# Performance work log

Measured on AMD Instinct MI355X. Metric: run time of the kernel, lower is better.

The kernel has to match this reference:

```python
import jax, jax.numpy as jnp
import numpy as np

T, D, H, L = 4096, 1024, 512, 2  # seq_len, input_size, per-direction hidden (state_size//2), num_layers


def setup_inputs() -> dict:
    key = jax.random.key(0)
    inp = {"emb": jax.random.normal(key, (T, D), jnp.float32) * 0.1}
    k = 1
    for d in ("fwd", "bwd"):
        for l in range(L):
            in_sz = D if l == 0 else H
            inp[f"{d}_Wih_{l}"] = jax.random.normal(jax.random.fold_in(key, k), (4 * H, in_sz), jnp.float32) * float(1.0 / np.sqrt(in_sz)); k += 1
            inp[f"{d}_Whh_{l}"] = jax.random.normal(jax.random.fold_in(key, k), (4 * H, H), jnp.float32) * float(1.0 / np.sqrt(H)); k += 1
            inp[f"{d}_bih_{l}"] = jnp.zeros((4 * H,), jnp.float32)
            inp[f"{d}_bhh_{l}"] = jnp.zeros((4 * H,), jnp.float32)
    return inp


def _lstm_stack(xs, params):
    """Run a stack of unidirectional LSTM layers over xs [T, in].
    Returns (final cells [L,H], final hiddens [L,H], top-layer outputs [T,H])."""
    cTs, hTs = [], []
    for Wih, Whh, bih, bhh in params:
        h0 = jnp.zeros((Wih.shape[0] // 4,), xs.dtype)

        def step(carry, x, Wih=Wih, Whh=Whh, b=bih + bhh):
            h, c = carry
            g = Wih @ x + Whh @ h + b          # [4H], torch LSTMCell gate order i,f,g,o
            i, f, gg, o = jnp.split(g, 4)
            c = jax.nn.sigmoid(f) * c + jax.nn.sigmoid(i) * jnp.tanh(gg)
            h = jax.nn.sigmoid(o) * jnp.tanh(c)
            return (h, c), h

        (hT, cT), xs = jax.lax.scan(step, (h0, h0), xs)
        cTs.append(cT)
        hTs.append(hT)
    return jnp.stack(cTs), jnp.stack(hTs), xs


def reference(emb,
              fwd_Wih_0, fwd_Whh_0, fwd_bih_0, fwd_bhh_0,
              fwd_Wih_1, fwd_Whh_1, fwd_bih_1, fwd_bhh_1,
              bwd_Wih_0, bwd_Whh_0, bwd_bih_0, bwd_bhh_0,
              bwd_Wih_1, bwd_Whh_1, bwd_bih_1, bwd_bhh_1):
    fparams = [(fwd_Wih_0, fwd_Whh_0, fwd_bih_0, fwd_bhh_0),
               (fwd_Wih_1, fwd_Whh_1, fwd_bih_1, fwd_bhh_1)]
    bparams = [(bwd_Wih_0, bwd_Whh_0, bwd_bih_0, bwd_bhh_0),
               (bwd_Wih_1, bwd_Whh_1, bwd_bih_1, bwd_bhh_1)]
    fc, fh, fy = _lstm_stack(emb, fparams)          # forward pass over sequence
    bc, bh, by = _lstm_stack(emb[::-1], bparams)    # backward pass over reversed sequence
    cell_memories = jnp.concatenate([fc, bc], axis=-1)   # [L, state_size]
    hidden_states = jnp.concatenate([fh, bh], axis=-1)   # [L, state_size]
    outputs = jnp.concatenate([fy, by[::-1]], axis=-1)   # [T, state_size] per-token final-layer states
    return (cell_memories, hidden_states, outputs)
```

## Files before the change

### kernel.cpp

```cpp
#include <hip/hip_runtime.h>
#include <cstdint>
#include <cstddef>

#define T_SEQ 4096
#define HSZ   512
#define NGATE 2048
#define DIN   1024
#define NB0   16
#define HB0   32
#define NB1   32
#define HB1   16
#define S_SLOT 16
#define CH    132

typedef unsigned long long u64;
typedef unsigned int u32;

__device__ __forceinline__ u64 exld(const u64* p) {
  return __hip_atomic_load(p, __ATOMIC_RELAXED, __HIP_MEMORY_SCOPE_AGENT);
}
__device__ __forceinline__ void exst(u64* p, u64 v) {
  __hip_atomic_store(p, v, __ATOMIC_RELAXED, __HIP_MEMORY_SCOPE_AGENT);
}
__device__ __forceinline__ int pgld(const u32* p) {
  return (int)__hip_atomic_load(p, __ATOMIC_RELAXED, __HIP_MEMORY_SCOPE_AGENT);
}
__device__ __forceinline__ void pgst(u32* p, u32 v) {
  __hip_atomic_store(p, v, __ATOMIC_RELAXED, __HIP_MEMORY_SCOPE_AGENT);
}

__device__ __forceinline__ float frcp(float x) { return __builtin_amdgcn_rcpf(x); }
__device__ __forceinline__ float fsig(float x) { return frcp(1.f + __expf(-x)); }
__device__ __forceinline__ float ftnh(float x) { return 1.f - 2.f * frcp(1.f + __expf(2.f * x)); }

__global__ void init_sync_kernel(u64* ex, u32* prog) {
  const int tid = blockIdx.x * blockDim.x + threadIdx.x;
  if (tid < 2 * 2 * S_SLOT * HSZ) exst(&ex[tid], 0ull);
  if (tid < 2 * (NB0 + NB1)) pgst(&prog[tid], 0u);
}

__global__ __launch_bounds__(256, 2)
void gemm_bias_kernel(const float* __restrict__ Xf, const float* __restrict__ Xb,
                      const float* __restrict__ Wf, const float* __restrict__ Wb,
                      const float* __restrict__ bif, const float* __restrict__ bhf,
                      const float* __restrict__ bib, const float* __restrict__ bhb,
                      float* __restrict__ Pf, float* __restrict__ Pb, int K)
{
  const int dir = blockIdx.z;
  const float* X  = dir ? Xb  : Xf;
  const float* W  = dir ? Wb  : Wf;
  const float* bi = dir ? bib : bif;
  const float* bh = dir ? bhb : bhf;
  float* P        = dir ? Pb  : Pf;

  const int m0 = blockIdx.x * 128;
  const int n0 = blockIdx.y * 128;
  const int tid = threadIdx.x;
  const int lr = tid >> 1;
  const int lk = (tid & 1) * 8;

  __shared__ float As[16*128];
  __shared__ float Bs[16*128];

  float acc[8][8];
  #pragma unroll
  for (int i = 0; i < 8; ++i)
    #pragma unroll
    for (int j = 0; j < 8; ++j) acc[i][j] = 0.f;

  for (int k0 = 0; k0 < K; k0 += 16) {
    const float4 a0 = *(const float4*)(X + (size_t)(m0+lr)*K + k0 + lk);
    const float4 a1 = *(const float4*)(X + (size_t)(m0+lr)*K + k0 + lk + 4);
    const float4 b0 = *(const float4*)(W + (size_t)(n0+lr)*K + k0 + lk);
    const float4 b1 = *(const float4*)(W + (size_t)(n0+lr)*K + k0 + lk + 4);
    __syncthreads();
    As[(lk+0)*128+lr]=a0.x; As[(lk+1)*128+lr]=a0.y; As[(lk+2)*128+lr]=a0.z; As[(lk+3)*128+lr]=a0.w;
    As[(lk+4)*128+lr]=a1.x; As[(lk+5)*128+lr]=a1.y; As[(lk+6)*128+lr]=a1.z; As[(lk+7)*128+lr]=a1.w;
    Bs[(lk+0)*128+lr]=b0.x; Bs[(lk+1)*128+lr]=b0.y; Bs[(lk+2)*128+lr]=b0.z; Bs[(lk+3)*128+lr]=b0.w;
    Bs[(lk+4)*128+lr]=b1.x; Bs[(lk+5)*128+lr]=b1.y; Bs[(lk+6)*128+lr]=b1.z; Bs[(lk+7)*128+lr]=b1.w;
    __syncthreads();
    #pragma unroll
    for (int kk = 0; kk < 16; ++kk) {
      const float4 A0 = *(const float4*)(As + kk*128 + (tid&15)*8);
      const float4 A1 = *(const float4*)(As + kk*128 + (tid&15)*8 + 4);
      const float4 B0 = *(const float4*)(Bs + kk*128 + (tid>>4)*8);
      const float4 B1 = *(const float4*)(Bs + kk*128 + (tid>>4)*8 + 4);
      const float av[8] = {A0.x,A0.y,A0.z,A0.w,A1.x,A1.y,A1.z,A1.w};
      const float bv[8] = {B0.x,B0.y,B0.z,B0.w,B1.x,B1.y,B1.z,B1.w};
      #pragma unroll
      for (int i = 0; i < 8; ++i)
        #pragma unroll
        for (int j = 0; j < 8; ++j) acc[i][j] += av[i]*bv[j];
    }
  }
  const int tm = m0 + (tid&15)*8;
  const int tn = n0 + (tid>>4)*8;
  #pragma unroll
  for (int i = 0; i < 8; ++i) {
    #pragma unroll
    for (int j = 0; j < 8; ++j) {
      const int n = tn + j;
      P[(size_t)(tm+i)*NGATE + n] = acc[i][j] + bi[n] + bh[n];
    }
  }
}

__global__ __launch_bounds__(512, 2)
void fused_recur_kernel(const float* __restrict__ Whh0_f, const float* __restrict__ Whh0_b,
                        const float* __restrict__ Wih1_f, const float* __restrict__ Whh1_f,
                        const float* __restrict__ bih1_f, const float* __restrict__ bhh1_f,
                        const float* __restrict__ Wih1_b, const float* __restrict__ Whh1_b,
                        const float* __restrict__ bih1_b, const float* __restrict__ bhh1_b,
                        const float* __restrict__ P_f, const float* __restrict__ P_b,
                        u64* ex0, u64* ex1, u32* prog0, u32* prog1,
                        float* __restrict__ out)
{
  const int bx  = blockIdx.x;
  const int tid = threadIdx.x;
  const int lane = tid & 63;
  const int wv   = tid >> 6;

  __shared__ float xh[2][8*CH];

  if (bx < 2*NB0) {
    const int dir = (bx >= NB0) ? 1 : 0;
    const int b   = bx - dir*NB0;
    const float* Whh = dir ? Whh0_b : Whh0_f;
    const float* P   = dir ? P_b    : P_f;
    u64* exS   = ex0 + (size_t)dir*S_SLOT*HSZ;
    u32* prS   = prog0 + dir*NB0;
    u32* prL1  = prog1 + dir*NB1;

    const int g  = lane & 3;
    const int el = (lane >> 2) & 3;
    const int cc = lane >> 4;
    const int e  = wv*4 + el;
    const int grow = g*HSZ + b*HB0 + e;
    const bool red0 = (cc == 0);
    const bool pub  = red0 && (g == 0);

    float4 w[32];
    {
      const float4* wp = (const float4*)(Whh + (size_t)grow*HSZ + cc*128);
      #pragma unroll
      for (int j = 0; j < 32; ++j) w[j] = wp[j];
    }

    float creg = 0.f;
    float pv = 0.f;
    if (red0) pv = P[(size_t)(dir ? (T_SEQ-1) : 0)*NGATE + grow];

    for (int t = 0; t < T_SEQ; ++t) {
      if ((t & 7) == 0) {
        if (tid >= 64 && tid < 64+NB0)       { while (pgld(&prS[tid-64])  < t-4) {} }
        else if (tid >= 96 && tid < 96+NB1)  { while (pgld(&prL1[tid-96]) < t-4) {} }
      }
      {
        const u64* sp = exS + (size_t)(t & (S_SLOT-1))*HSZ + tid;
        u64 v;
        do { v = exld(sp); } while ((u32)(v >> 32) != (u32)t);
        xh[t & 1][(tid>>7)*CH + (tid & 127)] = __uint_as_float((u32)v);
      }
      __syncthreads();
      if (tid == 0) pgst(&prS[b], (u32)(t+1));
      float pvn = 0.f;
      if (red0 && t+1 < T_SEQ) pvn = P[(size_t)(dir ? (T_SEQ-2-t) : (t+1))*NGATE + grow];
      const float4* h4 = (const float4*)(xh[t & 1] + cc*CH);
      float a0=0.f, a1=0.f, a2=0.f, a3=0.f;
      #pragma unroll
      for (int j = 0; j < 32; j += 4) {
        const float4 h0 = h4[j], h1 = h4[j+1], h2 = h4[j+2], h3 = h4[j+3];
        a0 += w[j].x*h0.x   + w[j].y*h0.y   + w[j].z*h0.z   + w[j].w*h0.w;
        a1 += w[j+1].x*h1.x + w[j+1].y*h1.y + w[j+1].z*h1.z + w[j+1].w*h1.w;
        a2 += w[j+2].x*h2.x + w[j+2].y*h2.y + w[j+2].z*h2.z + w[j+2].w*h2.w;
        a3 += w[j+3].x*h3.x + w[j+3].y*h3.y + w[j+3].z*h3.z + w[j+3].w*h3.w;
      }
      float acc = (a0+a1)+(a2+a3);
      acc += __shfl_xor(acc, 16);
      acc += __shfl_xor(acc, 32);
      const float val = acc + pv;
      pv = pvn;
      const float av = (g == 2) ? ftnh(val) : fsig(val);
      const float f1 = __shfl_xor(av, 1);
      const float f2 = __shfl_xor(av, 2);
      const float f3 = __shfl_xor(av, 3);
      if (pub) {
        creg = f1*creg + av*f2;
        const float hnew = f3*ftnh(creg);
        const int hidx = b*HB0 + e;
        const u64 pkt = ((u64)(u32)(t+1) << 32) | (u64)__float_as_uint(hnew);
        exst(exS + (size_t)((t+1) & (S_SLOT-1))*HSZ + hidx, pkt);
        if (t == T_SEQ-1) {
          out[dir*HSZ + hidx]        = creg;
          out[2048 + dir*HSZ + hidx] = hnew;
        }
      }
    }
  } else {
    const int r   = bx - 2*NB0;
    const int dir = (r >= NB1) ? 1 : 0;
    const int b   = r - dir*NB1;
    const float* Wih = dir ? Wih1_b : Wih1_f;
    const float* Whh = dir ? Whh1_b : Whh1_f;
    const float* bi  = dir ? bih1_b : bih1_f;
    const float* bh  = dir ? bhh1_b : bhh1_f;
    u64* exX = ex0 + (size_t)dir*S_SLOT*HSZ;
    u64* exS = ex1 + (size_t)dir*S_SLOT*HSZ;
    u32* prS = prog1 + dir*NB1;

    const int g   = lane & 3;
    const int el  = (lane >> 2) & 1;
    const int sub = lane >> 3;
    const int e   = wv*2 + el;
    const int grow = g*HSZ + b*HB1 + e;
    const bool red0 = (sub == 0);
    const bool pub  = red0 && (g == 0);

    float4 w[32];
    {
      const float* wsrc = (sub < 4) ? (Wih + (size_t)grow*HSZ + sub*128)
                                    : (Whh + (size_t)grow*HSZ + (sub-4)*128);
      const float4* wp = (const float4*)wsrc;
      #pragma unroll
      for (int j = 0; j < 32; ++j) w[j] = wp[j];
    }
    float brow = 0.f;
    if (red0) brow = bi[grow] + bh[grow];

    float creg = 0.f;
    u64 xpf = exld(exX + (size_t)(1 & (S_SLOT-1))*HSZ + tid);

    for (int t = 0; t < T_SEQ; ++t) {
      if ((t & 7) == 0 && tid >= 64 && tid < 64+NB1) { while (pgld(&prS[tid-64]) < t-4) {} }
      {
        const u64* px = exX + (size_t)((t+1) & (S_SLOT-1))*HSZ + tid;
        const u64* ph = exS + (size_t)(t & (S_SLOT-1))*HSZ + tid;
        u64 vx = xpf; bool okx = ((u32)(vx >> 32) == (u32)(t+1));
        float hv = 0.f; bool okh = false;
        do {
          if (!okx) { u64 v = exld(px); if ((u32)(v >> 32) == (u32)(t+1)) { vx = v; okx = true; } }
          if (!okh) { u64 v = exld(ph); if ((u32)(v >> 32) == (u32)t)     { hv = __uint_as_float((u32)v); okh = true; } }
        } while (!(okx && okh));
        xh[t & 1][(tid>>7)*CH + (tid & 127)]       = __uint_as_float((u32)vx);
        xh[t & 1][(4 + (tid>>7))*CH + (tid & 127)] = hv;
      }
      __syncthreads();
      if (tid == 0) pgst(&prS[b], (u32)(t+1));
      xpf = exld(exX + (size_t)((t+2) & (S_SLOT-1))*HSZ + tid);
      const float4* v4 = (const float4*)(xh[t & 1] + sub*CH);
      float a0=0.f, a1=0.f, a2=0.f, a3=0.f;
      #pragma unroll
      for (int j = 0; j < 32; j += 4) {
        const float4 h0 = v4[j], h1 = v4[j+1], h2 = v4[j+2], h3 = v4[j+3];
        a0 += w[j].x*h0.x   + w[j].y*h0.y   + w[j].z*h0.z   + w[j].w*h0.w;
        a1 += w[j+1].x*h1.x + w[j+1].y*h1.y + w[j+1].z*h1.z + w[j+1].w*h1.w;
        a2 += w[j+2].x*h2.x + w[j+2].y*h2.y + w[j+2].z*h2.z + w[j+2].w*h2.w;
        a3 += w[j+3].x*h3.x + w[j+3].y*h3.y + w[j+3].z*h3.z + w[j+3].w*h3.w;
      }
      float acc = (a0+a1)+(a2+a3);
      acc += __shfl_xor(acc, 8);
      acc += __shfl_xor(acc, 16);
      acc += __shfl_xor(acc, 32);
      const float val = acc + brow;
      const float av = (g == 2) ? ftnh(val) : fsig(val);
      const float f1 = __shfl_xor(av, 1);
      const float f2 = __shfl_xor(av, 2);
      const float f3 = __shfl_xor(av, 3);
      if (pub) {
        creg = f1*creg + av*f2;
        const float hnew = f3*ftnh(creg);
        const int hidx = b*HB1 + e;
        const u64 pkt = ((u64)(u32)(t+1) << 32) | (u64)__float_as_uint(hnew);
        exst(exS + (size_t)((t+1) & (S_SLOT-1))*HSZ + hidx, pkt);
        const int trow = dir ? (T_SEQ-1-t) : t;
        out[4096 + (size_t)trow*1024 + dir*HSZ + hidx] = hnew;
        if (t == T_SEQ-1) {
          out[1024 + dir*HSZ + hidx]        = creg;
          out[2048 + 1024 + dir*HSZ + hidx] = hnew;
        }
      }
    }
  }
}

extern "C" void kernel_launch(void* const* d_in, const int* in_sizes, int n_in,
                              void* d_out, int out_size, void* d_ws, size_t ws_size,
                              hipStream_t stream)
{
  const float* emb   = (const float*)d_in[0];
  const float* fWih0 = (const float*)d_in[1];
  const float* fWhh0 = (const float*)d_in[2];
  const float* fbih0 = (const float*)d_in[3];
  const float* fbhh0 = (const float*)d_in[4];
  const float* fWih1 = (const float*)d_in[5];
  const float* fWhh1 = (const float*)d_in[6];
  const float* fbih1 = (const float*)d_in[7];
  const float* fbhh1 = (const float*)d_in[8];
  const float* bWih0 = (const float*)d_in[9];
  const float* bWhh0 = (const float*)d_in[10];
  const float* bbih0 = (const float*)d_in[11];
  const float* bbhh0 = (const float*)d_in[12];
  const float* bWih1 = (const float*)d_in[13];
  const float* bWhh1 = (const float*)d_in[14];
  const float* bbih1 = (const float*)d_in[15];
  const float* bbhh1 = (const float*)d_in[16];
  float* out = (float*)d_out;

  float* P_f = (float*)d_ws;
  float* P_b = P_f + (size_t)T_SEQ*NGATE;
  u64*   ex0 = (u64*)(P_b + (size_t)T_SEQ*NGATE);
  u64*   ex1 = ex0 + 2*S_SLOT*HSZ;
  u32*   prog0 = (u32*)(ex1 + 2*S_SLOT*HSZ);
  u32*   prog1 = prog0 + 2*NB0;

  init_sync_kernel<<<32, 1024, 0, stream>>>(ex0, prog0);

  gemm_bias_kernel<<<dim3(32,16,2), 256, 0, stream>>>(
      emb, emb, fWih0, bWih0, fbih0, fbhh0, bbih0, bbhh0, P_f, P_b, DIN);

  fused_recur_kernel<<<96, 512, 0, stream>>>(
      fWhh0, bWhh0,
      fWih1, fWhh1, fbih1, fbhh1,
      bWih1, bWhh1, bbih1, bbhh1,
      P_f, P_b, ex0, ex1, prog0, prog1, out);
}
```

Before: 7.998 ms.

## Poll exchange buffers with wide 16-byte loads from fewer waves

Each polling thread now reads four tagged hidden-state values with dwordx4 inline-asm loads (sc0 sc1, cache-bypassing) instead of one 64-bit atomic load per thread. Polling is confined to the first 128 or 256 threads, so other waves skip it, and the progress-flag wait and publish move to wave 4. A fallback reverts to per-element atomic loads if 2048 wide-load attempts fail, since a 16-byte load is not guaranteed to be atomic. Launch bounds drop to one block per SM and an empty asm pins the weights in registers, trading occupancy for no register spills; the L1 next-step prefetch of x is removed.

```diff
diff --git a/kernel.cpp b/kernel.cpp
--- a/kernel.cpp
+++ b/kernel.cpp
@@ -27,6 +27,49 @@
 }
 __device__ __forceinline__ void pgst(u32* p, u32 v) {
   __hip_atomic_store(p, v, __ATOMIC_RELAXED, __HIP_MEMORY_SCOPE_AGENT);
+}
+
+__device__ __forceinline__ ulonglong2 exld16(const u64* p) {
+  ulonglong2 v;
+  asm volatile("global_load_dwordx4 %0, %1, off sc0 sc1\n"
+               "s_waitcnt vmcnt(0)"
+               : "=&v"(v) : "v"(p) : "memory");
+  return v;
+}
+__device__ __forceinline__ void exld16x2(const u64* p, ulonglong2& A, ulonglong2& B) {
+  asm volatile("global_load_dwordx4 %0, %2, off sc0 sc1\n"
+               "global_load_dwordx4 %1, %2, off offset:16 sc0 sc1\n"
+               "s_waitcnt vmcnt(0)"
+               : "=&v"(A), "=&v"(B) : "v"(p) : "memory");
+}
+
+__device__ __forceinline__ void poll4(const u64* base, u32 tag, bool& fast, float4& out) {
+  if (fast) {
+    ulonglong2 A, B; bool okA = false, okB = false; int it = 0;
+    while (!(okA && okB)) {
+      ulonglong2 nA, nB;
+      if (!okA && !okB) exld16x2(base, nA, nB);
+      else if (!okA)    nA = exld16(base);
+      else              nB = exld16(base + 2);
+      if (!okA && (u32)(nA.x >> 32) == tag && (u32)(nA.y >> 32) == tag) { A = nA; okA = true; }
+      if (!okB && (u32)(nB.x >> 32) == tag && (u32)(nB.y >> 32) == tag) { B = nB; okB = true; }
+      if (++it > 2048) { fast = false; break; }
+    }
+    if (okA && okB) {
+      out = make_float4(__uint_as_float((u32)A.x), __uint_as_float((u32)A.y),
+                        __uint_as_float((u32)B.x), __uint_as_float((u32)B.y));
+      return;
+    }
+  }
+  u64 v0=0, v1=0, v2=0, v3=0; bool o0=false, o1=false, o2=false, o3=false;
+  while (!(o0 && o1 && o2 && o3)) {
+    if (!o0) { u64 v = exld(base+0); if ((u32)(v>>32) == tag) { v0 = v; o0 = true; } }
+    if (!o1) { u64 v = exld(base+1); if ((u32)(v>>32) == tag) { v1 = v; o1 = true; } }
+    if (!o2) { u64 v = exld(base+2); if ((u32)(v>>32) == tag) { v2 = v; o2 = true; } }
+    if (!o3) { u64 v = exld(base+3); if ((u32)(v>>32) == tag) { v3 = v; o3 = true; } }
+  }
+  out = make_float4(__uint_as_float((u32)v0), __uint_as_float((u32)v1),
+                    __uint_as_float((u32)v2), __uint_as_float((u32)v3));
 }
 
 __device__ __forceinline__ float frcp(float x) { return __builtin_amdgcn_rcpf(x); }
@@ -105,7 +148,7 @@
   }
 }
 
-__global__ __launch_bounds__(512, 2)
+__global__ __launch_bounds__(512, 1)
 void fused_recur_kernel(const float* __restrict__ Whh0_f, const float* __restrict__ Whh0_b,
                         const float* __restrict__ Wih1_f, const float* __restrict__ Whh1_f,
                         const float* __restrict__ bih1_f, const float* __restrict__ bhh1_f,
@@ -145,24 +188,27 @@
       #pragma unroll
       for (int j = 0; j < 32; ++j) w[j] = wp[j];
     }
+    #pragma unroll
+    for (int j = 0; j < 32; ++j)
+      asm volatile("" : "+v"(w[j].x), "+v"(w[j].y), "+v"(w[j].z), "+v"(w[j].w));
 
     float creg = 0.f;
     float pv = 0.f;
     if (red0) pv = P[(size_t)(dir ? (T_SEQ-1) : 0)*NGATE + grow];
+    bool fastH = true;
 
     for (int t = 0; t < T_SEQ; ++t) {
       if ((t & 7) == 0) {
-        if (tid >= 64 && tid < 64+NB0)       { while (pgld(&prS[tid-64])  < t-4) {} }
-        else if (tid >= 96 && tid < 96+NB1)  { while (pgld(&prL1[tid-96]) < t-4) {} }
-      }
-      {
-        const u64* sp = exS + (size_t)(t & (S_SLOT-1))*HSZ + tid;
-        u64 v;
-        do { v = exld(sp); } while ((u32)(v >> 32) != (u32)t);
-        xh[t & 1][(tid>>7)*CH + (tid & 127)] = __uint_as_float((u32)v);
+        if (tid >= 256 && tid < 256+NB0)      { while (pgld(&prS[tid-256])  < t-4) {} }
+        else if (tid >= 288 && tid < 288+NB1) { while (pgld(&prL1[tid-288]) < t-4) {} }
+      }
+      if (tid < 128) {
+        float4 hv4;
+        poll4(exS + (size_t)(t & (S_SLOT-1))*HSZ + 4*tid, (u32)t, fastH, hv4);
+        *(float4*)&xh[t & 1][(tid>>5)*CH + 4*(tid&31)] = hv4;
       }
       __syncthreads();
-      if (tid == 0) pgst(&prS[b], (u32)(t+1));
+      if (tid == 256) pgst(&prS[b], (u32)(t+1));
       float pvn = 0.f;
       if (red0 && t+1 < T_SEQ) pvn = P[(size_t)(dir ? (T_SEQ-2-t) : (t+1))*NGATE + grow];
       const float4* h4 = (const float4*)(xh[t & 1] + cc*CH);
@@ -224,29 +270,30 @@
       #pragma unroll
       for (int j = 0; j < 32; ++j) w[j] = wp[j];
     }
+    #pragma unroll
+    for (int j = 0; j < 32; ++j)
+      asm volatile("" : "+v"(w[j].x), "+v"(w[j].y), "+v"(w[j].z), "+v"(w[j].w));
+
     float brow = 0.f;
     if (red0) brow = bi[grow] + bh[grow];
 
     float creg = 0.f;
-    u64 xpf = exld(exX + (size_t)(1 & (S_SLOT-1))*HSZ + tid);
+    bool fastX = true, fastH = true;
 
     for (int t = 0; t < T_SEQ; ++t) {
-      if ((t & 7) == 0 && tid >= 64 && tid < 64+NB1) { while (pgld(&prS[tid-64]) < t-4) {} }
-      {
-        const u64* px = exX + (size_t)((t+1) & (S_SLOT-1))*HSZ + tid;
-        const u64* ph = exS + (size_t)(t & (S_SLOT-1))*HSZ + tid;
-        u64 vx = xpf; bool okx = ((u32)(vx >> 32) == (u32)(t+1));
-        float hv = 0.f; bool okh = false;
-        do {
-          if (!okx) { u64 v = exld(px); if ((u32)(v >> 32) == (u32)(t+1)) { vx = v; okx = true; } }
-          if (!okh) { u64 v = exld(ph); if ((u32)(v >> 32) == (u32)t)     { hv = __uint_as_float((u32)v); okh = true; } }
-        } while (!(okx && okh));
-        xh[t & 1][(tid>>7)*CH + (tid & 127)]       = __uint_as_float((u32)vx);
-        xh[t & 1][(4 + (tid>>7))*CH + (tid & 127)] = hv;
+      if ((t & 7) == 0 && tid >= 256 && tid < 256+NB1) { while (pgld(&prS[tid-256]) < t-4) {} }
+      if (tid < 128) {
+        float4 xv4;
+        poll4(exX + (size_t)((t+1) & (S_SLOT-1))*HSZ + 4*tid, (u32)(t+1), fastX, xv4);
+        *(float4*)&xh[t & 1][(tid>>5)*CH + 4*(tid&31)] = xv4;
+      } else if (tid < 256) {
+        const int p2 = tid - 128;
+        float4 hv4;
+        poll4(exS + (size_t)(t & (S_SLOT-1))*HSZ + 4*p2, (u32)t, fastH, hv4);
+        *(float4*)&xh[t & 1][(4 + (p2>>5))*CH + 4*(p2&31)] = hv4;
       }
       __syncthreads();
-      if (tid == 0) pgst(&prS[b], (u32)(t+1));
-      xpf = exld(exX + (size_t)((t+2) & (S_SLOT-1))*HSZ + tid);
+      if (tid == 256) pgst(&prS[b], (u32)(t+1));
       const float4* v4 = (const float4*)(xh[t & 1] + sub*CH);
       float a0=0.f, a1=0.f, a2=0.f, a3=0.f;
       #pragma unroll
```

Result: slower. 12.23 ms (+52.9%).
